# Kernel tuning notes

Measured on AMD Instinct MI355X. Metric: run time of the kernel, lower is better.

Reference implementation:

```python
import jax, jax.numpy as jnp
import numpy as np

D = 1024      # embed_dim
H = 1365      # expert_hidden_dim = int(4096 / (select_top_k + num_shared_experts)) = int(4096/3)
E = 7         # num_experts = base_num_experts*factor - num_shared = 8 - 1
K = 2         # select_top_k
S_EXP = 1     # num_shared_experts
ALPHA = 0.01
C_Z = 0.001


def setup_inputs() -> dict:
    key = jax.random.key(0)
    ks = jax.random.split(key, 8)
    scaled = lambda k, shape, fan: jax.random.normal(k, shape, jnp.float32) * (1.0 / np.sqrt(fan))
    return {
        "x": jax.random.normal(ks[0], (4, 512, D), jnp.float32),
        "Wg": scaled(ks[1], (E, D), D),            # router weight (no bias)
        "W1": scaled(ks[2], (E, H, D), D),          # routed experts ffn[0] weight
        "b1": jnp.zeros((E, H), jnp.float32),
        "W2": scaled(ks[3], (E, D, H), H),          # routed experts ffn[3] weight
        "b2": jnp.zeros((E, D), jnp.float32),
        "Ws1": scaled(ks[4], (S_EXP, H, D), D),     # shared experts
        "bs1": jnp.zeros((S_EXP, H), jnp.float32),
        "Ws2": scaled(ks[5], (S_EXP, D, H), H),
        "bs2": jnp.zeros((S_EXP, D), jnp.float32),
    }


def _moe_forward(x, Wg, W1, b1, W2, b2, Ws1, bs1, Ws2, bs2):
    B, S, _ = x.shape
    xf = x.reshape(-1, D)                               # [N, D] flattened tokens
    N = xf.shape[0]

    # Gate (eval mode: no router noise, no dropout)
    logits = jnp.einsum('nd,ed->ne', xf, Wg)            # [N, E]
    dense_gate = jax.nn.softmax(logits, axis=-1)
    topk_logits, topk_idx = jax.lax.top_k(logits, K)    # [N, K]
    topk_w = jax.nn.softmax(topk_logits, axis=-1)       # [N, K]

    # Dense gate matrix: weight for selected experts, 0 elsewhere (equivalent to
    # the sorted dispatch + per-expert FFN + index_add combine in the original).
    gates = jnp.zeros((N, E), xf.dtype).at[jnp.arange(N)[:, None], topk_idx].set(topk_w)

    # Routed experts: exact GELU (approximate='none')
    h = jax.nn.gelu(jnp.einsum('nd,ehd->enh', xf, W1) + b1[:, None, :], approximate=False)  # [E, N, H]
    y = jnp.einsum('enh,edh->end', h, W2) + b2[:, None, :]                                  # [E, N, D]
    routed = jnp.einsum('ne,end->nd', gates, y)                                             # [N, D]

    # Shared experts (applied to every token, summed)
    hs = jax.nn.gelu(jnp.einsum('nd,shd->snh', xf, Ws1) + bs1[:, None, :], approximate=False)
    shared = jnp.einsum('snh,sdh->nd', hs, Ws2) + bs2.sum(0)

    final = (routed + shared).reshape(B, S, D)

    # Aux losses
    counts = jnp.zeros((E,), jnp.float32).at[topk_idx.reshape(-1)].add(1.0)  # bincount (non-diff, like torch long)
    dispatch_fraction = jax.lax.stop_gradient(counts) / (N * K)
    l_aux = ALPHA * E * jnp.sum(dispatch_fraction * dense_gate.mean(axis=0))
    cz_lz = C_Z * jnp.mean(jax.nn.logsumexp(logits, axis=-1) ** 2)
    return final, l_aux, cz_lz


def reference(x, Wg, W1, b1, W2, b2, Ws1, bs1, Ws2, bs2):
    return _moe_forward(x, Wg, W1, b1, W2, b2, Ws1, bs1, Ws2, bs2)
```

## Files before the change

### kernel.cpp

```cpp
#include <hip/hip_runtime.h>
#include <hip/hip_bf16.h>
#include <math.h>

typedef unsigned short u16;
typedef __attribute__((ext_vector_type(8))) short bf16x8;
typedef __attribute__((ext_vector_type(4))) float f32x4;

constexpr int D_ = 1024;
constexpr int H_ = 1365;
constexpr int E_ = 7;
constexpr int NTOK = 2048;
constexpr int HP = 1408;
constexpr int NE = 8;
constexpr int SHARED_BASE = 4096;
constexpr int SLOTS = 6144;

#define CI_COUNT 0
#define CI_OFF   8

constexpr size_t WS_CTRL = 0;
constexpr size_t WS_TIDX = 256;
constexpr size_t WS_TW   = WS_TIDX + (size_t)NTOK*2*4;
constexpr size_t WS_PROB = WS_TW   + (size_t)NTOK*2*4;
constexpr size_t WS_LSE2 = WS_PROB + (size_t)NTOK*8*4;
constexpr size_t WS_STOK = WS_LSE2 + (size_t)NTOK*4;
constexpr size_t WS_SW   = WS_STOK + (size_t)SLOTS*4;
constexpr size_t WS_B1   = WS_SW   + (size_t)SLOTS*4;
constexpr size_t WS_B2   = WS_B1   + (size_t)NE*H_*4;
constexpr size_t WS_XB   = ((WS_B2 + (size_t)NE*D_*4) + 255) & ~(size_t)255;
constexpr size_t WS_W1B  = WS_XB  + (size_t)NTOK*D_*2;
constexpr size_t WS_W2B  = WS_W1B + (size_t)NE*H_*D_*2;
constexpr size_t WS_HEB  = WS_W2B + (size_t)NE*D_*HP*2;

__device__ __forceinline__ u16 f2bf(float f) {
    __hip_bfloat16 h = __float2bfloat16(f);
    return __builtin_bit_cast(u16, h);
}

__device__ __forceinline__ void gload_lds16(const u16* g, u16* l) {
    __builtin_amdgcn_global_load_lds(
        (const __attribute__((address_space(1))) void*)g,
        (__attribute__((address_space(3))) void*)l, 16, 0, 0);
}

__device__ __forceinline__ uint4 pack8(float4 a, float4 b) {
    union { u16 h[8]; uint4 v; } u;
    u.h[0]=f2bf(a.x); u.h[1]=f2bf(a.y); u.h[2]=f2bf(a.z); u.h[3]=f2bf(a.w);
    u.h[4]=f2bf(b.x); u.h[5]=f2bf(b.y); u.h[6]=f2bf(b.z); u.h[7]=f2bf(b.w);
    return u.v;
}

__device__ __forceinline__ float fast_gelu(float v) {
    float u = 0.7978845608f * v * (1.f + 0.044715f * v * v);
    float e = __expf(2.f * u);
    float t = 1.f - 2.f / (e + 1.f);
    return 0.5f * v * (1.f + t);
}

#define BN 128
#define KSTEP 64
#define ASZ (64*KSTEP)
#define BSZ (128*KSTEP)

#define MFMA16(a,b,c) __builtin_amdgcn_mfma_f32_16x16x32_bf16(a, b, c, 0, 0, 0)

template<bool USE_STOK>
__device__ __forceinline__ void gemm1_body(u16* As, u16* Bs,
    const u16* xb, const u16* w1e, const float* b1e,
    const int* stok, int offset, int m0, int valid, int nt,
    u16* heb)
{
    int t = threadIdx.x, wid = t >> 6, lane = t & 63;
    int rl = lane >> 3, cl = lane & 7;
    int sg = cl ^ rl;

    int arow = wid*8 + rl;
    int ar = min(arow, valid-1);
    int tok = USE_STOK ? stok[offset + m0 + ar] : (m0 + ar);
    const u16* aP = xb + (size_t)tok*D_ + sg*8;
    int dOffA = wid*8*KSTEP;
    const u16* bP[2]; int dOffB[2];
    #pragma unroll
    for (int c = 0; c < 2; c++) {
        int brow = wid*16 + c*8 + rl;
        int jg = min(nt*BN + brow, H_-1);
        bP[c] = w1e + (size_t)jg*D_ + sg*8;
        dOffB[c] = (wid*16 + c*8)*KSTEP;
    }

    int wm = (wid >> 2)*32, wn = (wid & 3)*32;
    int frow = lane & 15, kgrp = lane >> 4, swz = frow & 7;
    f32x4 acc[2][2] = {};

    constexpr int nIter = D_/KSTEP;
    for (int tt = 0; tt < nIter; ++tt) {
        __syncthreads();
        int ko = tt*KSTEP;
        gload_lds16(aP+ko, As + dOffA);
        #pragma unroll
        for (int c = 0; c < 2; c++) gload_lds16(bP[c]+ko, Bs + dOffB[c]);
        __syncthreads();
        __builtin_amdgcn_s_setprio(1);
        #pragma unroll
        for (int s = 0; s < 2; s++) {
            int cc = ((s*4 + kgrp) ^ swz) * 8;
            bf16x8 af[2], bf[2];
            #pragma unroll
            for (int mf = 0; mf < 2; mf++)
                af[mf] = *(const bf16x8*)&As[(wm + mf*16 + frow)*KSTEP + cc];
            #pragma unroll
            for (int nf = 0; nf < 2; nf++)
                bf[nf] = *(const bf16x8*)&Bs[(wn + nf*16 + frow)*KSTEP + cc];
            #pragma unroll
            for (int mf = 0; mf < 2; mf++)
                #pragma unroll
                for (int nf = 0; nf < 2; nf++)
                    acc[mf][nf] = MFMA16(af[mf], bf[nf], acc[mf][nf]);
        }
        __builtin_amdgcn_s_setprio(0);
    }

    int r4 = (lane >> 4)*4, cEl = lane & 15;
    #pragma unroll
    for (int nf = 0; nf < 2; nf++) {
        int gcol = nt*BN + wn + nf*16 + cEl;
        bool cok = gcol < H_;
        float bias = cok ? b1e[gcol] : 0.f;
        #pragma unroll
        for (int mf = 0; mf < 2; mf++) {
            #pragma unroll
            for (int r = 0; r < 4; r++) {
                int row = wm + mf*16 + r4 + r;
                if (row < valid) {
                    float v = 0.f;
                    if (cok) v = fast_gelu(acc[mf][nf][r] + bias);
                    heb[(size_t)(offset + m0 + row)*HP + gcol] = f2bf(v);
                }
            }
        }
    }
}

template<int MODE>
__device__ __forceinline__ void gemm2_body(u16* As, u16* Bs,
    const u16* heb, const u16* w2e, const float* b2e, const float* sw,
    int offset, int m0, int valid, int nt, float* out, const int* stok)
{
    int t = threadIdx.x, wid = t >> 6, lane = t & 63;
    int rl = lane >> 3, cl = lane & 7;
    int sg = cl ^ rl;

    int arow = wid*8 + rl;
    int ar = min(arow, valid-1);
    const u16* aP = heb + (size_t)(offset + m0 + ar)*HP + sg*8;
    int dOffA = wid*8*KSTEP;
    const u16* bP[2]; int dOffB[2];
    #pragma unroll
    for (int c = 0; c < 2; c++) {
        int brow = wid*16 + c*8 + rl;
        int jg = nt*BN + brow;
        bP[c] = w2e + (size_t)jg*HP + sg*8;
        dOffB[c] = (wid*16 + c*8)*KSTEP;
    }

    int wm = (wid >> 2)*32, wn = (wid & 3)*32;
    int frow = lane & 15, kgrp = lane >> 4, swz = frow & 7;
    f32x4 acc[2][2] = {};

    constexpr int nIter = HP/KSTEP;
    for (int tt = 0; tt < nIter; ++tt) {
        __syncthreads();
        int ko = tt*KSTEP;
        gload_lds16(aP+ko, As + dOffA);
        #pragma unroll
        for (int c = 0; c < 2; c++) gload_lds16(bP[c]+ko, Bs + dOffB[c]);
        __syncthreads();
        __builtin_amdgcn_s_setprio(1);
        #pragma unroll
        for (int s = 0; s < 2; s++) {
            int cc = ((s*4 + kgrp) ^ swz) * 8;
            bf16x8 af[2], bf[2];
            #pragma unroll
            for (int mf = 0; mf < 2; mf++)
                af[mf] = *(const bf16x8*)&As[(wm + mf*16 + frow)*KSTEP + cc];
            #pragma unroll
            for (int nf = 0; nf < 2; nf++)
                bf[nf] = *(const bf16x8*)&Bs[(wn + nf*16 + frow)*KSTEP + cc];
            #pragma unroll
            for (int mf = 0; mf < 2; mf++)
                #pragma unroll
                for (int nf = 0; nf < 2; nf++)
                    acc[mf][nf] = MFMA16(af[mf], bf[nf], acc[mf][nf]);
        }
        __builtin_amdgcn_s_setprio(0);
    }

    int r4 = (lane >> 4)*4, cEl = lane & 15;
    #pragma unroll
    for (int nf = 0; nf < 2; nf++) {
        int gcol = nt*BN + wn + nf*16 + cEl;
        float bias = b2e[gcol];
        #pragma unroll
        for (int mf = 0; mf < 2; mf++) {
            #pragma unroll
            for (int r = 0; r < 4; r++) {
                int row = wm + mf*16 + r4 + r;
                if (row < valid) {
                    if (MODE == 0) {
                        out[(size_t)(m0 + row)*D_ + gcol] = acc[mf][nf][r] + bias;
                    } else {
                        int slot = offset + m0 + row;
                        atomicAdd(out + (size_t)stok[slot]*D_ + gcol,
                                  sw[slot]*(acc[mf][nf][r] + bias));
                    }
                }
            }
        }
    }
}

__device__ void finalize_body(char* big, char* small,
    const int* tidx, const float* tw, const float* probs, const float* lse2,
    int* ci, int* stok, float* sw, float* out)
{
    int*   lt   = (int*)big;
    float* psum = (float*)small;
    float* lsum = (float*)(small + 32);
    int*   cntS = (int*)(small + 64);
    int*   offS = (int*)(small + 96);
    int t = threadIdx.x;
    if (t < 8) { psum[t] = 0.f; cntS[t] = 0; }
    if (t == 0) *lsum = 0.f;
    for (int i = t; i < NTOK*2; i += 512) lt[i] = tidx[i];
    __syncthreads();
    float lp[E_] = {}; float ll = 0.f;
    for (int n = t; n < NTOK; n += 512) {
        #pragma unroll
        for (int e = 0; e < E_; e++) lp[e] += probs[n*8+e];
        ll += lse2[n];
    }
    #pragma unroll
    for (int e = 0; e < E_; e++) atomicAdd(&psum[e], lp[e]);
    atomicAdd(lsum, ll);
    int wid = t >> 6, lane = t & 63;
    if (wid < 7) {
        int c = 0;
        for (int i = lane; i < NTOK*2; i += 64) c += (lt[i] == wid) ? 1 : 0;
        #pragma unroll
        for (int m = 32; m >= 1; m >>= 1) c += __shfl_xor(c, m);
        if (lane == 0) cntS[wid] = c;
    } else {
        for (int n = lane; n < NTOK; n += 64) {
            stok[SHARED_BASE+n] = n; sw[SHARED_BASE+n] = 1.f;
        }
    }
    __syncthreads();
    if (t == 0) {
        int o = 0;
        for (int e = 0; e < E_; e++) { offS[e] = o; o += cntS[e]; }
        offS[7] = SHARED_BASE; cntS[7] = NTOK;
        float la = 0.f;
        for (int e = 0; e < E_; e++)
            la += ((float)cntS[e] / (float)(NTOK*2)) * (psum[e] / (float)NTOK);
        out[(size_t)NTOK*D_]     = 0.01f * 7.f * la;
        out[(size_t)NTOK*D_ + 1] = 0.001f * (*lsum) / (float)NTOK;
        #pragma unroll
        for (int e = 0; e < 8; e++) { ci[CI_COUNT+e] = cntS[e]; ci[CI_OFF+e] = offS[e]; }
    }
    __syncthreads();
    if (wid < 7) {
        int base = offS[wid], run = 0;
        for (int c0 = 0; c0 < NTOK*2; c0 += 64) {
            bool m = (lt[c0 + lane] == wid);
            unsigned long long bal = __ballot(m);
            int pre = __popcll(bal & ((1ull << lane) - 1ull));
            if (m) {
                int i = c0 + lane;
                int s = base + run + pre;
                stok[s] = i >> 1; sw[s] = tw[i];
            }
            run += __popcll(bal);
        }
    }
}

__global__ void prep_kernel(
    const float* __restrict__ x, const float* __restrict__ Wg,
    const float* __restrict__ W1, const float* __restrict__ Ws1,
    const float* __restrict__ b1, const float* __restrict__ bs1,
    int* __restrict__ tidx, float* __restrict__ tw,
    float* __restrict__ probs, float* __restrict__ lse2,
    u16* __restrict__ xb, u16* __restrict__ w1b, float* __restrict__ b1all)
{
    int b = blockIdx.x;
    if (b < 512) {
        int wid = threadIdx.x >> 6, lane = threadIdx.x & 63;
        int n = b*4 + wid;
        float p[E_] = {};
        const float* xr = x + (size_t)n*D_;
        u16* xbr = xb + (size_t)n*D_;
        #pragma unroll
        for (int j = 0; j < 4; j++) {
            int d0 = lane*4 + j*256;
            float4 xv = *(const float4*)(xr + d0);
            ushort4 h;
            h.x = f2bf(xv.x); h.y = f2bf(xv.y); h.z = f2bf(xv.z); h.w = f2bf(xv.w);
            *(ushort4*)(xbr + d0) = h;
            #pragma unroll
            for (int e = 0; e < E_; e++) {
                float4 wv = *(const float4*)(Wg + e*D_ + d0);
                p[e] += xv.x*wv.x + xv.y*wv.y + xv.z*wv.z + xv.w*wv.w;
            }
        }
        #pragma unroll
        for (int e = 0; e < E_; e++) {
            float v = p[e];
            #pragma unroll
            for (int m = 32; m >= 1; m >>= 1) v += __shfl_xor(v, m);
            p[e] = v;
        }
        if (lane == 0) {
            float mx = p[0];
            #pragma unroll
            for (int e = 1; e < E_; e++) mx = fmaxf(mx, p[e]);
            float pr[E_], sum = 0.f;
            #pragma unroll
            for (int e = 0; e < E_; e++) { pr[e] = __expf(p[e]-mx); sum += pr[e]; }
            float lse = mx + logf(sum);
            int i0 = 0;
            #pragma unroll
            for (int e = 1; e < E_; e++) if (p[e] > p[i0]) i0 = e;
            int i1 = -1;
            #pragma unroll
            for (int e = 0; e < E_; e++) if (e != i0 && (i1 < 0 || p[e] > p[i1])) i1 = e;
            float g = expf(p[i1] - p[i0]);
            tidx[n*2] = i0; tidx[n*2+1] = i1;
            tw[n*2] = 1.f/(1.f+g); tw[n*2+1] = g/(1.f+g);
            float inv = 1.f/sum;
            #pragma unroll
            for (int e = 0; e < E_; e++) probs[n*8+e] = pr[e]*inv;
            lse2[n] = lse*lse;
        }
        return;
    }
    const unsigned G1 = (unsigned)(NE*H_*D_/8);
    const unsigned NT = 1536u*256u;
    const unsigned W1FLAT = 7u*(unsigned)(H_*D_);
    unsigned tid = (unsigned)(b-512)*256u + threadIdx.x;
    unsigned i0 = tid, i1 = tid + NT, i2 = tid + 2u*NT, i3 = tid + 3u*NT;
    bool p3 = i3 < G1;
    float4 va0, vb0, va1, vb1, va2, vb2, va3, vb3;
    {
        const float* s0 = (i0*8u < W1FLAT) ? W1 + (size_t)i0*8u : Ws1 + ((size_t)i0*8u - W1FLAT);
        va0 = *(const float4*)s0; vb0 = *(const float4*)(s0+4);
        const float* s1 = (i1*8u < W1FLAT) ? W1 + (size_t)i1*8u : Ws1 + ((size_t)i1*8u - W1FLAT);
        va1 = *(const float4*)s1; vb1 = *(const float4*)(s1+4);
        const float* s2 = (i2*8u < W1FLAT) ? W1 + (size_t)i2*8u : Ws1 + ((size_t)i2*8u - W1FLAT);
        va2 = *(const float4*)s2; vb2 = *(const float4*)(s2+4);
        if (p3) {
            const float* s3 = (i3*8u < W1FLAT) ? W1 + (size_t)i3*8u : Ws1 + ((size_t)i3*8u - W1FLAT);
            va3 = *(const float4*)s3; vb3 = *(const float4*)(s3+4);
        }
    }
    ((uint4*)w1b)[i0] = pack8(va0, vb0);
    ((uint4*)w1b)[i1] = pack8(va1, vb1);
    ((uint4*)w1b)[i2] = pack8(va2, vb2);
    if (p3) ((uint4*)w1b)[i3] = pack8(va3, vb3);
    if (tid < 10920u) b1all[tid] = (tid < 9555u) ? b1[tid] : bs1[tid - 9555u];
}

__global__ __launch_bounds__(512, 8) void k2_kernel(
    const float* __restrict__ Ws2, const float* __restrict__ b2,
    const float* __restrict__ bs2,
    u16* __restrict__ w2b, float* __restrict__ b2all,
    const int* __restrict__ tidx, const float* __restrict__ tw,
    const float* __restrict__ probs, const float* __restrict__ lse2,
    int* __restrict__ ci, int* __restrict__ stok, float* __restrict__ sw,
    float* __restrict__ out,
    const u16* __restrict__ xb, const u16* __restrict__ w1b,
    const float* __restrict__ b1all, u16* __restrict__ heb)
{
    __shared__ u16 As[ASZ];
    __shared__ u16 Bs[BSZ];
    int b = blockIdx.x;
    if (b == 0) {
        finalize_body((char*)Bs, (char*)As, tidx, tw, probs, lse2, ci, stok, sw, out);
        return;
    }
    if (b <= 352) {
        int tdx = b - 1;
        int mt = tdx/11, nt = tdx - mt*11;
        gemm1_body<false>(As, Bs, xb, w1b + (size_t)7*H_*D_, b1all + 7*H_,
                          nullptr, SHARED_BASE, mt*64, 64, nt, heb);
        return;
    }
    unsigned tid = (unsigned)(b-353)*512u + threadIdx.x;
    if (tid < 8192u) b2all[tid] = (tid < 7168u) ? b2[tid] : bs2[tid - 7168u];
    int lane = threadIdx.x & 63;
    int rs0 = (((b-353)*8) + (threadIdx.x >> 6)) * 2;
    #pragma unroll
    for (int j = 0; j < 2; j++) {
        int rs = rs0 + j;
        const float* src = Ws2 + (size_t)rs*(size_t)H_;
        u16* dst = w2b + (size_t)(7*D_ + rs)*HP;
        #pragma unroll
        for (int h0 = 0; h0 < HP; h0 += 64) {
            int h = h0 + lane;
            float v = (h < H_) ? src[h] : 0.f;
            dst[h] = f2bf(v);
        }
    }
}

__global__ __launch_bounds__(512, 8) void k3_kernel(
    const int* __restrict__ ci, const int* __restrict__ stok,
    const u16* __restrict__ xb, const u16* __restrict__ w1b,
    const float* __restrict__ b1all, u16* __restrict__ heb,
    const float* __restrict__ W2, u16* __restrict__ w2b,
    const u16* __restrict__ w2b_c, const float* __restrict__ b2all,
    float* __restrict__ out)
{
    __shared__ u16 As[ASZ];
    __shared__ u16 Bs[BSZ];
    int x = blockIdx.x, yb = blockIdx.y;
    if (yb < 352) {
        if (x == 7) return;
        int e = x, mt = yb/11, nt = yb - mt*11;
        int count = ci[CI_COUNT+e];
        int m0 = mt*64;
        if (m0 >= count) return;
        gemm1_body<true>(As, Bs, xb, w1b + (size_t)e*H_*D_, b1all + e*H_,
                         stok, ci[CI_OFF+e], m0, min(64, count-m0), nt, heb);
    } else if (yb < 384) {
        int idx = (yb - 352)*8 + x;
        int mt = idx >> 3, nt = idx & 7;
        gemm2_body<0>(As, Bs, heb, w2b_c + (size_t)7*D_*HP, b2all + 7*D_,
                      nullptr, SHARED_BASE, mt*64, 64, nt, out, nullptr);
    } else {
        int idx = (yb - 384)*8 + x;
        int lane = threadIdx.x & 63;
        int rw0 = idx*16 + (threadIdx.x >> 6)*2;
        #pragma unroll
        for (int j = 0; j < 2; j++) {
            int rw = rw0 + j;
            int ec = rw >> 10, drow = rw & 1023;
            const float* src = W2 + ((size_t)ec*D_ + drow)*(size_t)H_;
            u16* dst = w2b + (size_t)rw*HP;
            #pragma unroll
            for (int h0 = 0; h0 < HP; h0 += 64) {
                int h = h0 + lane;
                float v = (h < H_) ? src[h] : 0.f;
                dst[h] = f2bf(v);
            }
        }
    }
}

__global__ __launch_bounds__(512, 8) void k4_kernel(
    const int* __restrict__ ci, const int* __restrict__ stok, const float* __restrict__ sw,
    const u16* __restrict__ heb, const u16* __restrict__ w2b,
    const float* __restrict__ b2all, float* __restrict__ out)
{
    __shared__ u16 As[ASZ];
    __shared__ u16 Bs[BSZ];
    int x = blockIdx.x;
    if (x == 7) return;
    int yb = blockIdx.y;
    int e = x, mt = yb >> 3, nt = yb & 7;
    int count = ci[CI_COUNT+e];
    int m0 = mt*64;
    if (m0 >= count) return;
    gemm2_body<1>(As, Bs, heb, w2b + (size_t)e*D_*HP, b2all + e*D_,
                  sw, ci[CI_OFF+e], m0, min(64, count-m0), nt, out, stok);
}

extern "C" void kernel_launch(void* const* d_in, const int* in_sizes, int n_in,
                              void* d_out, int out_size, void* d_ws, size_t ws_size,
                              hipStream_t stream)
{
    const float* x   = (const float*)d_in[0];
    const float* Wg  = (const float*)d_in[1];
    const float* W1  = (const float*)d_in[2];
    const float* b1  = (const float*)d_in[3];
    const float* W2  = (const float*)d_in[4];
    const float* b2  = (const float*)d_in[5];
    const float* Ws1 = (const float*)d_in[6];
    const float* bs1 = (const float*)d_in[7];
    const float* Ws2 = (const float*)d_in[8];
    const float* bs2 = (const float*)d_in[9];
    float* out = (float*)d_out;
    char* ws = (char*)d_ws;

    int*   ci    = (int*)(ws + WS_CTRL);
    int*   tidx  = (int*)(ws + WS_TIDX);
    float* tw    = (float*)(ws + WS_TW);
    float* probs = (float*)(ws + WS_PROB);
    float* lse2  = (float*)(ws + WS_LSE2);
    int*   stok  = (int*)(ws + WS_STOK);
    float* sw    = (float*)(ws + WS_SW);
    float* b1all = (float*)(ws + WS_B1);
    float* b2all = (float*)(ws + WS_B2);
    u16*   xb    = (u16*)(ws + WS_XB);
    u16*   w1b   = (u16*)(ws + WS_W1B);
    u16*   w2b   = (u16*)(ws + WS_W2B);
    u16*   heb   = (u16*)(ws + WS_HEB);

    prep_kernel<<<2048, 256, 0, stream>>>(x, Wg, W1, Ws1, b1, bs1,
                                          tidx, tw, probs, lse2, xb, w1b, b1all);
    k2_kernel<<<417, 512, 0, stream>>>(Ws2, b2, bs2, w2b, b2all,
                                       tidx, tw, probs, lse2, ci, stok, sw, out,
                                       xb, w1b, b1all, heb);
    k3_kernel<<<dim3(8, 352 + 32 + 56), 512, 0, stream>>>(ci, stok, xb, w1b, b1all, heb,
                                                          W2, w2b, w2b, b2all, out);
    k4_kernel<<<dim3(8, 256), 512, 0, stream>>>(ci, stok, sw, heb, w2b, b2all, out);
}
```

Baseline: 127.2 us.

## Double-buffer LDS tiles in expert GEMM main loops to overlap loads with MFMA

Both GEMM bodies now prefetch the next K-slice into a second LDS buffer while computing on the current one, replacing the two-barrier load-then-compute loop with a single wait and barrier per iteration. Shared arrays are doubled and launch bounds lowered from 8 to 6 to match the larger LDS footprint. The aim is to hide global-to-LDS latency behind matrix math. In exchange the kernel runs fewer resident blocks per CU, and the vmcnt(0) wait at the end of each iteration still serialises on the prefetch, which limits how much overlap is possible.

```diff
diff --git a/kernel.cpp b/kernel.cpp
--- a/kernel.cpp
+++ b/kernel.cpp
@@ -92,14 +92,24 @@
     int frow = lane & 15, kgrp = lane >> 4, swz = frow & 7;
     f32x4 acc[2][2] = {};
 
+    gload_lds16(aP, As + dOffA);
+    #pragma unroll
+    for (int c = 0; c < 2; c++) gload_lds16(bP[c], Bs + dOffB[c]);
+    asm volatile("s_waitcnt vmcnt(0)" ::: "memory");
+    __syncthreads();
+
     constexpr int nIter = D_/KSTEP;
+    int cur = 0;
     for (int tt = 0; tt < nIter; ++tt) {
-        __syncthreads();
-        int ko = tt*KSTEP;
-        gload_lds16(aP+ko, As + dOffA);
-        #pragma unroll
-        for (int c = 0; c < 2; c++) gload_lds16(bP[c]+ko, Bs + dOffB[c]);
-        __syncthreads();
+        if (tt + 1 < nIter) {
+            int ko = (tt+1)*KSTEP;
+            gload_lds16(aP+ko, As + (cur^1)*ASZ + dOffA);
+            #pragma unroll
+            for (int c = 0; c < 2; c++)
+                gload_lds16(bP[c]+ko, Bs + (cur^1)*BSZ + dOffB[c]);
+        }
+        const u16* ab = As + cur*ASZ;
+        const u16* bb = Bs + cur*BSZ;
         __builtin_amdgcn_s_setprio(1);
         #pragma unroll
         for (int s = 0; s < 2; s++) {
@@ -107,10 +117,10 @@
             bf16x8 af[2], bf[2];
             #pragma unroll
             for (int mf = 0; mf < 2; mf++)
-                af[mf] = *(const bf16x8*)&As[(wm + mf*16 + frow)*KSTEP + cc];
+                af[mf] = *(const bf16x8*)&ab[(wm + mf*16 + frow)*KSTEP + cc];
             #pragma unroll
             for (int nf = 0; nf < 2; nf++)
-                bf[nf] = *(const bf16x8*)&Bs[(wn + nf*16 + frow)*KSTEP + cc];
+                bf[nf] = *(const bf16x8*)&bb[(wn + nf*16 + frow)*KSTEP + cc];
             #pragma unroll
             for (int mf = 0; mf < 2; mf++)
                 #pragma unroll
@@ -118,6 +128,9 @@
                     acc[mf][nf] = MFMA16(af[mf], bf[nf], acc[mf][nf]);
         }
         __builtin_amdgcn_s_setprio(0);
+        asm volatile("s_waitcnt vmcnt(0)" ::: "memory");
+        __syncthreads();
+        cur ^= 1;
     }
 
     int r4 = (lane >> 4)*4, cEl = lane & 15;
@@ -167,14 +180,24 @@
     int frow = lane & 15, kgrp = lane >> 4, swz = frow & 7;
     f32x4 acc[2][2] = {};
 
+    gload_lds16(aP, As + dOffA);
+    #pragma unroll
+    for (int c = 0; c < 2; c++) gload_lds16(bP[c], Bs + dOffB[c]);
+    asm volatile("s_waitcnt vmcnt(0)" ::: "memory");
+    __syncthreads();
+
     constexpr int nIter = HP/KSTEP;
+    int cur = 0;
     for (int tt = 0; tt < nIter; ++tt) {
-        __syncthreads();
-        int ko = tt*KSTEP;
-        gload_lds16(aP+ko, As + dOffA);
-        #pragma unroll
-        for (int c = 0; c < 2; c++) gload_lds16(bP[c]+ko, Bs + dOffB[c]);
-        __syncthreads();
+        if (tt + 1 < nIter) {
+            int ko = (tt+1)*KSTEP;
+            gload_lds16(aP+ko, As + (cur^1)*ASZ + dOffA);
+            #pragma unroll
+            for (int c = 0; c < 2; c++)
+                gload_lds16(bP[c]+ko, Bs + (cur^1)*BSZ + dOffB[c]);
+        }
+        const u16* ab = As + cur*ASZ;
+        const u16* bb = Bs + cur*BSZ;
         __builtin_amdgcn_s_setprio(1);
         #pragma unroll
         for (int s = 0; s < 2; s++) {
@@ -182,10 +205,10 @@
             bf16x8 af[2], bf[2];
             #pragma unroll
             for (int mf = 0; mf < 2; mf++)
-                af[mf] = *(const bf16x8*)&As[(wm + mf*16 + frow)*KSTEP + cc];
+                af[mf] = *(const bf16x8*)&ab[(wm + mf*16 + frow)*KSTEP + cc];
             #pragma unroll
             for (int nf = 0; nf < 2; nf++)
-                bf[nf] = *(const bf16x8*)&Bs[(wn + nf*16 + frow)*KSTEP + cc];
+                bf[nf] = *(const bf16x8*)&bb[(wn + nf*16 + frow)*KSTEP + cc];
             #pragma unroll
             for (int mf = 0; mf < 2; mf++)
                 #pragma unroll
@@ -193,6 +216,9 @@
                     acc[mf][nf] = MFMA16(af[mf], bf[nf], acc[mf][nf]);
         }
         __builtin_amdgcn_s_setprio(0);
+        asm volatile("s_waitcnt vmcnt(0)" ::: "memory");
+        __syncthreads();
+        cur ^= 1;
     }
 
     int r4 = (lane >> 4)*4, cEl = lane & 15;
@@ -369,7 +395,7 @@
     if (tid < 10920u) b1all[tid] = (tid < 9555u) ? b1[tid] : bs1[tid - 9555u];
 }
 
-__global__ __launch_bounds__(512, 8) void k2_kernel(
+__global__ __launch_bounds__(512, 6) void k2_kernel(
     const float* __restrict__ Ws2, const float* __restrict__ b2,
     const float* __restrict__ bs2,
     u16* __restrict__ w2b, float* __restrict__ b2all,
@@ -380,8 +406,8 @@
     const u16* __restrict__ xb, const u16* __restrict__ w1b,
     const float* __restrict__ b1all, u16* __restrict__ heb)
 {
-    __shared__ u16 As[ASZ];
-    __shared__ u16 Bs[BSZ];
+    __shared__ u16 As[2*ASZ];
+    __shared__ u16 Bs[2*BSZ];
     int b = blockIdx.x;
     if (b == 0) {
         finalize_body((char*)Bs, (char*)As, tidx, tw, probs, lse2, ci, stok, sw, out);
@@ -412,7 +438,7 @@
     }
 }
 
-__global__ __launch_bounds__(512, 8) void k3_kernel(
+__global__ __launch_bounds__(512, 6) void k3_kernel(
     const int* __restrict__ ci, const int* __restrict__ stok,
     const u16* __restrict__ xb, const u16* __restrict__ w1b,
     const float* __restrict__ b1all, u16* __restrict__ heb,
@@ -420,8 +446,8 @@
     const u16* __restrict__ w2b_c, const float* __restrict__ b2all,
     float* __restrict__ out)
 {
-    __shared__ u16 As[ASZ];
-    __shared__ u16 Bs[BSZ];
+    __shared__ u16 As[2*ASZ];
+    __shared__ u16 Bs[2*BSZ];
     int x = blockIdx.x, yb = blockIdx.y;
     if (yb < 352) {
         if (x == 7) return;
@@ -456,13 +482,13 @@
     }
 }
 
-__global__ __launch_bounds__(512, 8) void k4_kernel(
+__global__ __launch_bounds__(512, 6) void k4_kernel(
     const int* __restrict__ ci, const int* __restrict__ stok, const float* __restrict__ sw,
     const u16* __restrict__ heb, const u16* __restrict__ w2b,
     const float* __restrict__ b2all, float* __restrict__ out)
 {
-    __shared__ u16 As[ASZ];
-    __shared__ u16 Bs[BSZ];
+    __shared__ u16 As[2*ASZ];
+    __shared__ u16 Bs[2*BSZ];
     int x = blockIdx.x;
     if (x == 7) return;
     int yb = blockIdx.y;
```

New measurement: 127.3 us. No clear change (+0.0%).

## Fuse W1 fp32-to-bf16 conversion into GEMM1 tile loads

Applied to the files above, without the earlier changes.

Drops the separate prep pass that converted all of W1/Ws1 to bf16 in workspace. GEMM1 now reads the fp32 weights directly, converts them to bf16 in registers and writes swizzled tiles into LDS. This removes a full read and write of the 8x1365x1024 weights plus the extra bf16 reread. The cost is that fp32 weight tiles are reloaded once per token tile, up to 32 m-tiles for the shared expert, and the async global-to-LDS path is replaced by synchronous register loads.

```diff
diff --git a/kernel.cpp b/kernel.cpp
--- a/kernel.cpp
+++ b/kernel.cpp
@@ -28,8 +28,7 @@
 constexpr size_t WS_B1   = WS_SW   + (size_t)SLOTS*4;
 constexpr size_t WS_B2   = WS_B1   + (size_t)NE*H_*4;
 constexpr size_t WS_XB   = ((WS_B2 + (size_t)NE*D_*4) + 255) & ~(size_t)255;
-constexpr size_t WS_W1B  = WS_XB  + (size_t)NTOK*D_*2;
-constexpr size_t WS_W2B  = WS_W1B + (size_t)NE*H_*D_*2;
+constexpr size_t WS_W2B  = WS_XB  + (size_t)NTOK*D_*2;
 constexpr size_t WS_HEB  = WS_W2B + (size_t)NE*D_*HP*2;
 
 __device__ __forceinline__ u16 f2bf(float f) {
@@ -66,7 +65,7 @@
 
 template<bool USE_STOK>
 __device__ __forceinline__ void gemm1_body(u16* As, u16* Bs,
-    const u16* xb, const u16* w1e, const float* b1e,
+    const u16* xb, const float* w1f, const float* b1e,
     const int* stok, int offset, int m0, int valid, int nt,
     u16* heb)
 {
@@ -79,14 +78,12 @@
     int tok = USE_STOK ? stok[offset + m0 + ar] : (m0 + ar);
     const u16* aP = xb + (size_t)tok*D_ + sg*8;
     int dOffA = wid*8*KSTEP;
-    const u16* bP[2]; int dOffB[2];
-    #pragma unroll
-    for (int c = 0; c < 2; c++) {
-        int brow = wid*16 + c*8 + rl;
-        int jg = min(nt*BN + brow, H_-1);
-        bP[c] = w1e + (size_t)jg*D_ + sg*8;
-        dOffB[c] = (wid*16 + c*8)*KSTEP;
-    }
+
+    int brow = t >> 2, q = t & 3;
+    int jg = min(nt*BN + brow, H_-1);
+    const float* bSrc = w1f + (size_t)jg*D_ + q*16;
+    u16* bDst0 = Bs + brow*KSTEP + (((q*2)     ^ (brow & 7)) * 8);
+    u16* bDst1 = Bs + brow*KSTEP + (((q*2 + 1) ^ (brow & 7)) * 8);
 
     int wm = (wid >> 2)*32, wn = (wid & 3)*32;
     int frow = lane & 15, kgrp = lane >> 4, swz = frow & 7;
@@ -97,13 +94,15 @@
         __syncthreads();
         int ko = tt*KSTEP;
         gload_lds16(aP+ko, As + dOffA);
-        #pragma unroll
-        for (int c = 0; c < 2; c++) gload_lds16(bP[c]+ko, Bs + dOffB[c]);
+        const float4* s = (const float4*)(bSrc + ko);
+        float4 f0 = s[0], f1 = s[1], f2 = s[2], f3 = s[3];
+        *(uint4*)bDst0 = pack8(f0, f1);
+        *(uint4*)bDst1 = pack8(f2, f3);
         __syncthreads();
         __builtin_amdgcn_s_setprio(1);
         #pragma unroll
-        for (int s = 0; s < 2; s++) {
-            int cc = ((s*4 + kgrp) ^ swz) * 8;
+        for (int sI = 0; sI < 2; sI++) {
+            int cc = ((sI*4 + kgrp) ^ swz) * 8;
             bf16x8 af[2], bf[2];
             #pragma unroll
             for (int mf = 0; mf < 2; mf++)
@@ -286,11 +285,10 @@
 
 __global__ void prep_kernel(
     const float* __restrict__ x, const float* __restrict__ Wg,
-    const float* __restrict__ W1, const float* __restrict__ Ws1,
     const float* __restrict__ b1, const float* __restrict__ bs1,
     int* __restrict__ tidx, float* __restrict__ tw,
     float* __restrict__ probs, float* __restrict__ lse2,
-    u16* __restrict__ xb, u16* __restrict__ w1b, float* __restrict__ b1all)
+    u16* __restrict__ xb, float* __restrict__ b1all)
 {
     int b = blockIdx.x;
     if (b < 512) {
@@ -343,42 +341,20 @@
         }
         return;
     }
-    const unsigned G1 = (unsigned)(NE*H_*D_/8);
-    const unsigned NT = 1536u*256u;
-    const unsigned W1FLAT = 7u*(unsigned)(H_*D_);
     unsigned tid = (unsigned)(b-512)*256u + threadIdx.x;
-    unsigned i0 = tid, i1 = tid + NT, i2 = tid + 2u*NT, i3 = tid + 3u*NT;
-    bool p3 = i3 < G1;
-    float4 va0, vb0, va1, vb1, va2, vb2, va3, vb3;
-    {
-        const float* s0 = (i0*8u < W1FLAT) ? W1 + (size_t)i0*8u : Ws1 + ((size_t)i0*8u - W1FLAT);
-        va0 = *(const float4*)s0; vb0 = *(const float4*)(s0+4);
-        const float* s1 = (i1*8u < W1FLAT) ? W1 + (size_t)i1*8u : Ws1 + ((size_t)i1*8u - W1FLAT);
-        va1 = *(const float4*)s1; vb1 = *(const float4*)(s1+4);
-        const float* s2 = (i2*8u < W1FLAT) ? W1 + (size_t)i2*8u : Ws1 + ((size_t)i2*8u - W1FLAT);
-        va2 = *(const float4*)s2; vb2 = *(const float4*)(s2+4);
-        if (p3) {
-            const float* s3 = (i3*8u < W1FLAT) ? W1 + (size_t)i3*8u : Ws1 + ((size_t)i3*8u - W1FLAT);
-            va3 = *(const float4*)s3; vb3 = *(const float4*)(s3+4);
-        }
-    }
-    ((uint4*)w1b)[i0] = pack8(va0, vb0);
-    ((uint4*)w1b)[i1] = pack8(va1, vb1);
-    ((uint4*)w1b)[i2] = pack8(va2, vb2);
-    if (p3) ((uint4*)w1b)[i3] = pack8(va3, vb3);
     if (tid < 10920u) b1all[tid] = (tid < 9555u) ? b1[tid] : bs1[tid - 9555u];
 }
 
 __global__ __launch_bounds__(512, 8) void k2_kernel(
-    const float* __restrict__ Ws2, const float* __restrict__ b2,
-    const float* __restrict__ bs2,
+    const float* __restrict__ Ws1, const float* __restrict__ Ws2,
+    const float* __restrict__ b2, const float* __restrict__ bs2,
     u16* __restrict__ w2b, float* __restrict__ b2all,
     const int* __restrict__ tidx, const float* __restrict__ tw,
     const float* __restrict__ probs, const float* __restrict__ lse2,
     int* __restrict__ ci, int* __restrict__ stok, float* __restrict__ sw,
     float* __restrict__ out,
-    const u16* __restrict__ xb, const u16* __restrict__ w1b,
-    const float* __restrict__ b1all, u16* __restrict__ heb)
+    const u16* __restrict__ xb, const float* __restrict__ b1all,
+    u16* __restrict__ heb)
 {
     __shared__ u16 As[ASZ];
     __shared__ u16 Bs[BSZ];
@@ -390,7 +366,7 @@
     if (b <= 352) {
         int tdx = b - 1;
         int mt = tdx/11, nt = tdx - mt*11;
-        gemm1_body<false>(As, Bs, xb, w1b + (size_t)7*H_*D_, b1all + 7*H_,
+        gemm1_body<false>(As, Bs, xb, Ws1, b1all + 7*H_,
                           nullptr, SHARED_BASE, mt*64, 64, nt, heb);
         return;
     }
@@ -414,7 +390,7 @@
 
 __global__ __launch_bounds__(512, 8) void k3_kernel(
     const int* __restrict__ ci, const int* __restrict__ stok,
-    const u16* __restrict__ xb, const u16* __restrict__ w1b,
+    const u16* __restrict__ xb, const float* __restrict__ W1,
     const float* __restrict__ b1all, u16* __restrict__ heb,
     const float* __restrict__ W2, u16* __restrict__ w2b,
     const u16* __restrict__ w2b_c, const float* __restrict__ b2all,
@@ -429,7 +405,7 @@
         int count = ci[CI_COUNT+e];
         int m0 = mt*64;
         if (m0 >= count) return;
-        gemm1_body<true>(As, Bs, xb, w1b + (size_t)e*H_*D_, b1all + e*H_,
+        gemm1_body<true>(As, Bs, xb, W1 + (size_t)e*H_*D_, b1all + e*H_,
                          stok, ci[CI_OFF+e], m0, min(64, count-m0), nt, heb);
     } else if (yb < 384) {
         int idx = (yb - 352)*8 + x;
@@ -501,16 +477,15 @@
     float* b1all = (float*)(ws + WS_B1);
     float* b2all = (float*)(ws + WS_B2);
     u16*   xb    = (u16*)(ws + WS_XB);
-    u16*   w1b   = (u16*)(ws + WS_W1B);
     u16*   w2b   = (u16*)(ws + WS_W2B);
     u16*   heb   = (u16*)(ws + WS_HEB);
 
-    prep_kernel<<<2048, 256, 0, stream>>>(x, Wg, W1, Ws1, b1, bs1,
-                                          tidx, tw, probs, lse2, xb, w1b, b1all);
-    k2_kernel<<<417, 512, 0, stream>>>(Ws2, b2, bs2, w2b, b2all,
+    prep_kernel<<<560, 256, 0, stream>>>(x, Wg, b1, bs1,
+                                         tidx, tw, probs, lse2, xb, b1all);
+    k2_kernel<<<417, 512, 0, stream>>>(Ws1, Ws2, b2, bs2, w2b, b2all,
                                        tidx, tw, probs, lse2, ci, stok, sw, out,
-                                       xb, w1b, b1all, heb);
-    k3_kernel<<<dim3(8, 352 + 32 + 56), 512, 0, stream>>>(ci, stok, xb, w1b, b1all, heb,
+                                       xb, b1all, heb);
+    k3_kernel<<<dim3(8, 352 + 32 + 56), 512, 0, stream>>>(ci, stok, xb, W1, b1all, heb,
                                                           W2, w2b, w2b, b2all, out);
     k4_kernel<<<dim3(8, 256), 512, 0, stream>>>(ci, stok, sw, heb, w2b, b2all, out);
 }
```

New measurement: 140.5 us. 1.1x slower.
